# Kernel optimization log

Hardware: AMD Instinct MI355X
Metric: run time of the kernel (lower is better)

The kernel has to match this reference:

```python
import jax, jax.numpy as jnp
import numpy as np

D_MODEL = 1024
N_HEADS = 16
N_GROUPS = 4
D_HEAD = D_MODEL // N_HEADS  # 64
HPG = N_HEADS // N_GROUPS    # heads per KV group = 4
B, T = 2, 2048


def _rope(x):
    # x: [B, H, T, D]; interleaved even/odd rotary, matching the torch module
    t, d = x.shape[2], x.shape[3]
    pos = jnp.arange(t, dtype=jnp.float32)[:, None]                      # [T,1]
    freq = jnp.exp(-(jnp.arange(0, d, 2, dtype=jnp.float32) / d)
                   * jnp.log(jnp.float32(10000.0)))                      # [D/2]
    angle = pos * freq                                                   # [T, D/2]
    cos, sin = jnp.cos(angle), jnp.sin(angle)
    xe, xo = x[..., ::2], x[..., 1::2]
    re = xe * cos - xo * sin
    ro = xe * sin + xo * cos
    return jnp.stack([re, ro], axis=-1).reshape(x.shape)


def setup_inputs() -> dict:
    key = jax.random.key(0)
    ks = jax.random.split(key, 10)
    s = 0.02
    return {
        "x":  jax.random.normal(ks[0], (B, T, D_MODEL), dtype=jnp.float32),
        "Wq": jax.random.normal(ks[1], (D_MODEL, D_MODEL), dtype=jnp.float32) * s,
        "bq": jax.random.normal(ks[2], (D_MODEL,), dtype=jnp.float32) * s,
        "Wk": jax.random.normal(ks[3], (D_MODEL, N_GROUPS * D_HEAD), dtype=jnp.float32) * s,
        "bk": jax.random.normal(ks[4], (N_GROUPS * D_HEAD,), dtype=jnp.float32) * s,
        "Wv": jax.random.normal(ks[5], (D_MODEL, N_GROUPS * D_HEAD), dtype=jnp.float32) * s,
        "bv": jax.random.normal(ks[6], (N_GROUPS * D_HEAD,), dtype=jnp.float32) * s,
        "Wo": jax.random.normal(ks[7], (D_MODEL, D_MODEL), dtype=jnp.float32) * s,
        "bo": jax.random.normal(ks[8], (D_MODEL,), dtype=jnp.float32) * s,
    }


def reference(x, Wq, bq, Wk, bk, Wv, bv, Wo, bo):
    b, t, _ = x.shape
    q = (x @ Wq + bq).reshape(b, t, N_HEADS, D_HEAD).transpose(0, 2, 1, 3)    # [B,H,T,D]
    k = (x @ Wk + bk).reshape(b, t, N_GROUPS, D_HEAD).transpose(0, 2, 1, 3)   # [B,G,T,D]
    v = (x @ Wv + bv).reshape(b, t, N_GROUPS, D_HEAD).transpose(0, 2, 1, 3)
    # GQA broadcast: idx = arange(n_heads) // heads_per_group  ==  repeat each group HPG times
    k = jnp.repeat(k, HPG, axis=1)                                            # [B,H,T,D]
    v = jnp.repeat(v, HPG, axis=1)
    q = _rope(q)
    k = _rope(k)
    scale = jnp.float32(np.sqrt(D_HEAD))
    scores = jnp.einsum('bhtd,bhsd->bhts', q, k) / scale                      # [B,H,T,T]
    causal = jnp.tril(jnp.ones((t, t), dtype=bool))
    scores = jnp.where(causal, scores, -jnp.inf)
    probs = jax.nn.softmax(scores, axis=-1)
    # dropout(p=0.05) is identity in eval mode
    attn = jnp.einsum('bhts,bhsd->bhtd', probs, v)
    out = attn.transpose(0, 2, 1, 3).reshape(b, t, N_HEADS * D_HEAD)
    return out @ Wo + bo
```

## Files before the change

### kernel.cpp

```cpp
#include <hip/hip_runtime.h>
#include <stdint.h>

typedef unsigned short u16;
typedef __attribute__((ext_vector_type(4))) float f32x4;
typedef __attribute__((ext_vector_type(8))) short bf16x8;
typedef __attribute__((ext_vector_type(4))) short bf16x4;

#define T_SEQ 2048
#define DM 1024
#define NH 16
#define NG 4
#define DH 64
#define QSCALE 0.18033688011112042f

__device__ __forceinline__ u16 f2bf(float f) {
    union { float f; uint32_t u; } v; v.f = f;
    uint32_t r = (v.u + 0x7FFFu + ((v.u >> 16) & 1u)) >> 16;
    return (u16)r;
}
__device__ __forceinline__ float bf2f(u16 u) {
    union { uint32_t u; float f; } v; v.u = ((uint32_t)u) << 16;
    return v.f;
}
__device__ __forceinline__ float fexp2(float x) {
#if __has_builtin(__builtin_amdgcn_exp2f)
    return __builtin_amdgcn_exp2f(x);
#else
    return exp2f(x);
#endif
}
__device__ __forceinline__ uint32_t cvtpk_bf16(float a, float b) {
    uint32_t r;
    asm("v_cvt_pk_bf16_f32 %0, %1, %2" : "=v"(r) : "v"(a), "v"(b));
    return r;
}

#if __has_builtin(__builtin_amdgcn_mfma_f32_16x16x16_bf16)
__device__ __forceinline__ f32x4 mfma16(bf16x4 a, bf16x4 b, f32x4 c) {
    return __builtin_amdgcn_mfma_f32_16x16x16_bf16(a, b, c, 0, 0, 0);
}
#elif __has_builtin(__builtin_amdgcn_mfma_f32_16x16x16bf16_1k)
__device__ __forceinline__ f32x4 mfma16(bf16x4 a, bf16x4 b, f32x4 c) {
    return __builtin_amdgcn_mfma_f32_16x16x16bf16_1k(a, b, c, 0, 0, 0);
}
#else
__device__ __forceinline__ f32x4 mfma16(bf16x4 a, bf16x4 b, f32x4 c) {
    asm("v_mfma_f32_16x16x16_bf16 %0, %1, %2, %0" : "+v"(c) : "v"(a), "v"(b));
    return c;
}
#endif

__device__ __forceinline__ void async16(const void* g, void* l) {
    __builtin_amdgcn_global_load_lds(
        (const __attribute__((address_space(1))) void*)g,
        (__attribute__((address_space(3))) void*)l,
        16, 0, 0);
}

__global__ __launch_bounds__(256) void k_prep(
    const float* __restrict__ x, u16* __restrict__ xb,
    const float* __restrict__ Wq, const float* __restrict__ Wk,
    const float* __restrict__ Wv, const float* __restrict__ Wo,
    u16* __restrict__ wqkvt, u16* __restrict__ wot,
    const float* __restrict__ bq, const float* __restrict__ bk,
    const float* __restrict__ bv, float* __restrict__ bqkv,
    float2* __restrict__ tbl) {
    int blk = blockIdx.x;
    int tid = threadIdx.x;
    if (blk < 2048) {
        int i = blk * 256 + tid;
        const float4* p = (const float4*)x + (size_t)i * 2;
        float4 a = p[0], b = p[1];
        bf16x8 v;
        v[0] = (short)f2bf(a.x); v[1] = (short)f2bf(a.y);
        v[2] = (short)f2bf(a.z); v[3] = (short)f2bf(a.w);
        v[4] = (short)f2bf(b.x); v[5] = (short)f2bf(b.y);
        v[6] = (short)f2bf(b.z); v[7] = (short)f2bf(b.w);
        ((bf16x8*)xb)[i] = v;
        return;
    }
    int t = blk - 2048;
    if (t >= 2560) {
        int u = t - 2560;
        if (u < 6) {
            int i = u * 256 + tid;
            if (i < 1536) {
                float v;
                if (i < 1024) v = bq[i];
                else if (i < 1280) v = bk[i - 1024];
                else v = bv[i - 1280];
                bqkv[i] = v;
            }
        } else {
            int idx = (u - 6) * 256 + tid;
            int tt = idx >> 5, i = idx & 31;
            float freq = exp2f(-(float)i * (13.287712379549449f / 32.0f));
            float ang = (float)tt * freq;
            tbl[idx] = make_float2(cosf(ang), sinf(ang));
        }
        return;
    }
    const float* src; u16* dst; int N;
    if (t < 1024)      { src = Wq; dst = wqkvt;                      N = 1024; }
    else if (t < 1280) { t -= 1024; src = Wk; dst = wqkvt + (size_t)1024 * 1024; N = 256; }
    else if (t < 1536) { t -= 1280; src = Wv; dst = wqkvt + (size_t)1280 * 1024; N = 256; }
    else               { t -= 1536; src = Wo; dst = wot;             N = 1024; }
    int ntiles = N >> 5;
    int n0 = (t % ntiles) * 32, k0 = (t / ntiles) * 32;
    __shared__ float tile[32][33];
    int tx = tid & 31, ty = tid >> 5;
#pragma unroll
    for (int q = 0; q < 4; q++)
        tile[ty + q * 8][tx] = src[(size_t)(k0 + ty + q * 8) * N + n0 + tx];
    __syncthreads();
#pragma unroll
    for (int q = 0; q < 4; q++)
        dst[(size_t)(n0 + ty + q * 8) * 1024 + k0 + tx] = f2bf(tile[tx][ty + q * 8]);
}

__global__ __launch_bounds__(256) void k_gemm_qkv(
    const u16* __restrict__ A, const u16* __restrict__ Bt,
    const float* __restrict__ bias, const float2* __restrict__ tbl,
    u16* __restrict__ Qo, u16* __restrict__ Ko, u16* __restrict__ Vto) {
    const int K = 1024;
    __shared__ __align__(16) u16 As[64 * 64];
    __shared__ __align__(16) u16 Bs[128 * 64];
    int tid = threadIdx.x;
    int lane = tid & 63, wid = tid >> 6;
    int wr = wid >> 1, wc = wid & 1;
    int l15 = lane & 15, lhi = lane >> 4;
    int row0 = blockIdx.y * 64, col0 = blockIdx.x * 128;
    f32x4 acc[2][4] = {};

    for (int k0 = 0; k0 < K; k0 += 64) {
#pragma unroll
        for (int i = 0; i < 2; i++) {
            int c = i * 256 + tid;
            int r = c >> 3, ch = c & 7;
            int sch = ch ^ (r & 7);
            async16(A + (size_t)(row0 + r) * K + k0 + sch * 8, &As[c * 8]);
        }
#pragma unroll
        for (int i = 0; i < 4; i++) {
            int c = i * 256 + tid;
            int r = c >> 3, ch = c & 7;
            int sch = ch ^ (r & 7);
            async16(Bt + (size_t)(col0 + r) * K + k0 + sch * 8, &Bs[c * 8]);
        }
        __syncthreads();
#pragma unroll
        for (int ks = 0; ks < 2; ks++) {
            bf16x8 af[2], bfr[4];
#pragma unroll
            for (int m = 0; m < 2; m++) {
                int r = wr * 32 + m * 16 + l15;
                int kb = (ks * 64 + lhi * 16) ^ ((r & 7) << 4);
                af[m] = *(const bf16x8*)((const char*)As + r * 128 + kb);
            }
#pragma unroll
            for (int n = 0; n < 4; n++) {
                int r = wc * 64 + n * 16 + l15;
                int kb = (ks * 64 + lhi * 16) ^ ((r & 7) << 4);
                bfr[n] = *(const bf16x8*)((const char*)Bs + r * 128 + kb);
            }
#pragma unroll
            for (int m = 0; m < 2; m++)
#pragma unroll
                for (int n = 0; n < 4; n++)
                    acc[m][n] = __builtin_amdgcn_mfma_f32_16x16x32_bf16(
                        af[m], bfr[n], acc[m][n], 0, 0, 0);
        }
        __syncthreads();
    }

    int type = (col0 >= 1280) ? 2 : (col0 >= 1024 ? 1 : 0);
    int rbase = row0 + wr * 32;
#pragma unroll
    for (int n = 0; n < 4; n++) {
        int col = col0 + wc * 64 + n * 16 + l15;
        float bv = bias[col];
        if (type == 2) {
            int cc = col - 1280;
            int g = cc >> 6, d = cc & 63;
#pragma unroll
            for (int m = 0; m < 2; m++)
#pragma unroll
                for (int i = 0; i < 4; i++) {
                    int rowg = rbase + m * 16 + lhi * 4 + i;
                    int t = rowg & (T_SEQ - 1), b = rowg >> 11;
                    int sp = t ^ ((d & 1) << 2);
                    Vto[(((size_t)(b * NG + g)) * DH + d) * T_SEQ + sp] =
                        f2bf(acc[m][n][i] + bv);
                }
        } else {
            float ssgn = (col & 1) ? 1.f : -1.f;
            int ip = (col & 63) >> 1;
#pragma unroll
            for (int m = 0; m < 2; m++)
#pragma unroll
                for (int i = 0; i < 4; i++) {
                    int rowg = rbase + m * 16 + lhi * 4 + i;
                    int t = rowg & (T_SEQ - 1), b = rowg >> 11;
                    float v = acc[m][n][i] + bv;
                    float other = __shfl_xor(v, 1);
                    float2 cs = tbl[t * 32 + ip];
                    float out = v * cs.x + other * cs.y * ssgn;
                    if (type == 0) {
                        int h = col >> 6, d = col & 63;
                        Qo[(((size_t)(b * NH + h)) * T_SEQ + t) * DH + d] =
                            f2bf(out * QSCALE);
                    } else {
                        int cc = col - 1024;
                        int g = cc >> 6, d = cc & 63;
                        Ko[(((size_t)(b * NG + g)) * T_SEQ + t) * DH + d] = f2bf(out);
                    }
                }
        }
    }
}

__global__ __launch_bounds__(256) void k_gemm_out(
    const u16* __restrict__ A, const u16* __restrict__ Bt,
    const float* __restrict__ bias, float* __restrict__ C,
    int M, int N, int K) {
    __shared__ __align__(16) u16 As[64 * 64];
    __shared__ __align__(16) u16 Bs[128 * 64];
    int tid = threadIdx.x;
    int lane = tid & 63, wid = tid >> 6;
    int wr = wid >> 1, wc = wid & 1;
    int l15 = lane & 15, lhi = lane >> 4;
    int row0 = blockIdx.y * 64, col0 = blockIdx.x * 128;
    f32x4 acc[2][4] = {};

    for (int k0 = 0; k0 < K; k0 += 64) {
#pragma unroll
        for (int i = 0; i < 2; i++) {
            int c = i * 256 + tid;
            int r = c >> 3, ch = c & 7;
            int sch = ch ^ (r & 7);
            async16(A + (size_t)(row0 + r) * K + k0 + sch * 8, &As[c * 8]);
        }
#pragma unroll
        for (int i = 0; i < 4; i++) {
            int c = i * 256 + tid;
            int r = c >> 3, ch = c & 7;
            int sch = ch ^ (r & 7);
            async16(Bt + (size_t)(col0 + r) * K + k0 + sch * 8, &Bs[c * 8]);
        }
        __syncthreads();
#pragma unroll
        for (int ks = 0; ks < 2; ks++) {
            bf16x8 af[2], bfr[4];
#pragma unroll
            for (int m = 0; m < 2; m++) {
                int r = wr * 32 + m * 16 + l15;
                int kb = (ks * 64 + lhi * 16) ^ ((r & 7) << 4);
                af[m] = *(const bf16x8*)((const char*)As + r * 128 + kb);
            }
#pragma unroll
            for (int n = 0; n < 4; n++) {
                int r = wc * 64 + n * 16 + l15;
                int kb = (ks * 64 + lhi * 16) ^ ((r & 7) << 4);
                bfr[n] = *(const bf16x8*)((const char*)Bs + r * 128 + kb);
            }
#pragma unroll
            for (int m = 0; m < 2; m++)
#pragma unroll
                for (int n = 0; n < 4; n++)
                    acc[m][n] = __builtin_amdgcn_mfma_f32_16x16x32_bf16(
                        af[m], bfr[n], acc[m][n], 0, 0, 0);
        }
        __syncthreads();
    }
#pragma unroll
    for (int n = 0; n < 4; n++) {
        int col = col0 + wc * 64 + n * 16 + l15;
        float bv = bias[col];
#pragma unroll
        for (int m = 0; m < 2; m++) {
            int row = row0 + wr * 32 + m * 16 + lhi * 4;
#pragma unroll
            for (int i = 0; i < 4; i++)
                C[(size_t)(row + i) * N + col] = acc[m][n][i] + bv;
        }
    }
}

__global__ __launch_bounds__(256) void k_attn(
    const u16* __restrict__ Q, const u16* __restrict__ K,
    const u16* __restrict__ Vt, u16* __restrict__ Aout) {
    int i0 = blockIdx.x;
    int u = i0 >> 5;
    int qt = (u < 16) ? (31 - u) : (u - 16);
    int bh = i0 & 31;
    int b = bh >> 4, h = bh & 15, g = h >> 2;
    int tid = threadIdx.x;
    int lane = tid & 63, wid = tid >> 6;
    int l15 = lane & 15, lhi = lane >> 4;

    const u16* Kp = K + ((size_t)(b * NG + g)) * T_SEQ * DH;
    const u16* Vp = Vt + ((size_t)(b * NG + g)) * DH * T_SEQ;

    __shared__ __align__(16) u16 Ks[2][64 * 64];
    __shared__ __align__(16) u16 Vs[2][64 * 64];

    const u16* Qp = Q + ((size_t)bh * T_SEQ + qt * 64) * DH;
    bf16x8 qf[2];
#pragma unroll
    for (int ks = 0; ks < 2; ks++)
        qf[ks] = *(const bf16x8*)(Qp + (size_t)(wid * 16 + l15) * DH + ks * 32 + lhi * 8);

    f32x4 of[4] = {};
    float m_i = -3.0e38f, l_i = 0.f;

    int nt = qt + 1;
    int swz = (l15 & 7) << 4;

    int c0 = tid, c1 = tid + 256;
    int rk0 = c0 >> 3, rk1 = c1 >> 3;
    int sk0 = (c0 & 7) ^ (rk0 & 7);
    int sk1 = (c1 & 7) ^ (rk1 & 7);
    int sv0 = (c0 & 7) ^ ((rk0 >> 1) & 7);
    int sv1 = (c1 & 7) ^ ((rk1 >> 1) & 7);
    const u16* kg0 = Kp + rk0 * DH + sk0 * 8;
    const u16* kg1 = Kp + rk1 * DH + sk1 * 8;
    const u16* vg0 = Vp + (size_t)rk0 * T_SEQ + sv0 * 8;
    const u16* vg1 = Vp + (size_t)rk1 * T_SEQ + sv1 * 8;

    async16(kg0, &Ks[0][c0 * 8]);
    async16(kg1, &Ks[0][c1 * 8]);
    async16(vg0, &Vs[0][c0 * 8]);
    async16(vg1, &Vs[0][c1 * 8]);
    __syncthreads();

#pragma unroll 1
    for (int it = 0; it < nt; it++) {
        int cur = it & 1;
        if (it + 1 < nt) {
            int nx = cur ^ 1;
            int ko = (it + 1) << 12;
            int vo = (it + 1) << 6;
            async16(kg0 + ko, &Ks[nx][c0 * 8]);
            async16(kg1 + ko, &Ks[nx][c1 * 8]);
            async16(vg0 + vo, &Vs[nx][c0 * 8]);
            async16(vg1 + vo, &Vs[nx][c1 * 8]);
        }
        const u16* Kc = Ks[cur];
        const u16* Vc = Vs[cur];

        f32x4 sf[4] = {};
        __builtin_amdgcn_s_setprio(1);
#pragma unroll
        for (int ks = 0; ks < 2; ks++)
#pragma unroll
            for (int n = 0; n < 4; n++) {
                int kb = (ks * 64 + lhi * 16) ^ swz;
                bf16x8 kf = *(const bf16x8*)((const char*)Kc + (n * 16 + l15) * 128 + kb);
                sf[n] = __builtin_amdgcn_mfma_f32_16x16x32_bf16(kf, qf[ks], sf[n], 0, 0, 0);
            }
        __builtin_amdgcn_s_setprio(0);

        if (it == nt - 1) {
            int qrow = qt * 64 + wid * 16 + l15;
            int sb = it * 64 + lhi * 4;
#pragma unroll
            for (int n = 0; n < 4; n++)
#pragma unroll
                for (int i = 0; i < 4; i++)
                    if (sb + n * 16 + i > qrow) sf[n][i] = -3.0e38f;
        }

        float pmt = sf[0][0];
#pragma unroll
        for (int n = 0; n < 4; n++)
#pragma unroll
            for (int i = 0; i < 4; i++)
                pmt = fmaxf(pmt, sf[n][i]);
        if (!__all(pmt - m_i <= 8.f)) {
#pragma unroll
            for (int off = 16; off <= 32; off <<= 1)
                pmt = fmaxf(pmt, __shfl_xor(pmt, off));
            float mn = fmaxf(m_i, pmt);
            float sc = fexp2(m_i - mn);
            m_i = mn;
            l_i *= sc;
            float sc4[4];
#pragma unroll
            for (int i = 0; i < 4; i++)
                sc4[i] = __shfl(sc, lhi * 4 + i);
#pragma unroll
            for (int n = 0; n < 4; n++)
#pragma unroll
                for (int i = 0; i < 4; i++)
                    of[n][i] *= sc4[i];
        }
        bf16x4 pa[4];
#pragma unroll
        for (int n = 0; n < 4; n++) {
#pragma unroll
            for (int i = 0; i < 4; i++) {
                float p = fexp2(sf[n][i] - m_i);
                sf[n][i] = p;
                l_i += p;
            }
            union { uint32_t u[2]; bf16x4 v; } pu;
            pu.u[0] = cvtpk_bf16(sf[n][0], sf[n][1]);
            pu.u[1] = cvtpk_bf16(sf[n][2], sf[n][3]);
            pa[n] = pu.v;
        }

        __builtin_amdgcn_s_setprio(1);
#pragma unroll
        for (int nd = 0; nd < 4; nd++) {
            int rowb = (nd * 16 + l15) * 128;
#pragma unroll
            for (int n = 0; n < 4; n++) {
                int kb = ((4 * n + lhi) ^ l15) << 3;
                bf16x4 vf = *(const bf16x4*)((const char*)Vc + rowb + kb);
                of[nd] = mfma16(pa[n], vf, of[nd]);
            }
        }
        __builtin_amdgcn_s_setprio(0);
        __syncthreads();
    }

#pragma unroll
    for (int off = 16; off <= 32; off <<= 1)
        l_i += __shfl_xor(l_i, off);
    float lq[4];
#pragma unroll
    for (int i = 0; i < 4; i++)
        lq[i] = __shfl(l_i, lhi * 4 + i);
#pragma unroll
    for (int n = 0; n < 4; n++)
#pragma unroll
        for (int i = 0; i < 4; i++) {
            int trow = qt * 64 + wid * 16 + lhi * 4 + i;
            float v = of[n][i] / lq[i];
            Aout[((size_t)(b * T_SEQ + trow)) * DM + h * 64 + n * 16 + l15] = f2bf(v);
        }
}

extern "C" void kernel_launch(void* const* d_in, const int* in_sizes, int n_in,
                              void* d_out, int out_size, void* d_ws, size_t ws_size,
                              hipStream_t stream) {
    const float* x  = (const float*)d_in[0];
    const float* Wq = (const float*)d_in[1];
    const float* bq = (const float*)d_in[2];
    const float* Wk = (const float*)d_in[3];
    const float* bk = (const float*)d_in[4];
    const float* Wv = (const float*)d_in[5];
    const float* bv = (const float*)d_in[6];
    const float* Wo = (const float*)d_in[7];
    const float* bo = (const float*)d_in[8];

    char* ws = (char*)d_ws;
    size_t o = 0;
    u16*   xb    = (u16*)(ws + o);  o += (size_t)4096 * 1024 * 2;
    u16*   wqkvt = (u16*)(ws + o);  o += (size_t)1536 * 1024 * 2;
    u16*   wot   = (u16*)(ws + o);  o += (size_t)1024 * 1024 * 2;
    float* bqkv  = (float*)(ws + o); o += 1536 * 4;
    o = (o + 255) & ~(size_t)255;
    u16*   Qb    = (u16*)(ws + o);  o += (size_t)2 * NH * T_SEQ * DH * 2;
    u16*   Kb    = (u16*)(ws + o);  o += (size_t)2 * NG * T_SEQ * DH * 2;
    u16*   Vtb   = (u16*)(ws + o);  o += (size_t)2 * NG * DH * T_SEQ * 2;
    u16*   attnb = (u16*)(ws + o);  o += (size_t)4096 * 1024 * 2;
    float2* tbl  = (float2*)(ws + o); o += (size_t)2048 * 32 * 8;

    k_prep<<<4870, 256, 0, stream>>>(x, xb, Wq, Wk, Wv, Wo, wqkvt, wot, bq, bk, bv, bqkv, tbl);
    k_gemm_qkv<<<dim3(12, 64), 256, 0, stream>>>(xb, wqkvt, bqkv, tbl, Qb, Kb, Vtb);
    k_attn<<<1024, 256, 0, stream>>>(Qb, Kb, Vtb, attnb);
    k_gemm_out<<<dim3(8, 64), 256, 0, stream>>>(attnb, wot, bo, (float*)d_out, 4096, 1024, 1024);
}
```

Baseline: 91.30 us.

## Double-buffer LDS tiles in projection GEMMs and unify them into one template

The QKV and output projection GEMMs are merged into one templated kernel, with the epilogue chosen by a template parameter. The main loop now double-buffers the A and B shared-memory tiles: the next K-tile's async global-to-LDS copies are issued before the MFMA work on the current tile, so load latency overlaps compute. Global source pointers are also precomputed once, outside the loop. In exchange, shared memory per block doubles, which may lower occupancy. The attention kernel only gets a variable rename.

```diff
diff --git a/kernel.cpp b/kernel.cpp
--- a/kernel.cpp
+++ b/kernel.cpp
@@ -118,13 +118,14 @@
         dst[(size_t)(n0 + ty + q * 8) * 1024 + k0 + tx] = f2bf(tile[tx][ty + q * 8]);
 }
 
-__global__ __launch_bounds__(256) void k_gemm_qkv(
+template <int EPI>
+__global__ __launch_bounds__(256) void k_gemm(
     const u16* __restrict__ A, const u16* __restrict__ Bt,
-    const float* __restrict__ bias, const float2* __restrict__ tbl,
-    u16* __restrict__ Qo, u16* __restrict__ Ko, u16* __restrict__ Vto) {
-    const int K = 1024;
-    __shared__ __align__(16) u16 As[64 * 64];
-    __shared__ __align__(16) u16 Bs[128 * 64];
+    const float* __restrict__ bias, float* __restrict__ C,
+    const float2* __restrict__ tbl, u16* __restrict__ Qo,
+    u16* __restrict__ Ko, u16* __restrict__ Vto, int N, int K) {
+    __shared__ __align__(16) u16 As[2][64 * 64];
+    __shared__ __align__(16) u16 Bs[2][128 * 64];
     int tid = threadIdx.x;
     int lane = tid & 63, wid = tid >> 6;
     int wr = wid >> 1, wc = wid & 1;
@@ -132,22 +133,37 @@
     int row0 = blockIdx.y * 64, col0 = blockIdx.x * 128;
     f32x4 acc[2][4] = {};
 
-    for (int k0 = 0; k0 < K; k0 += 64) {
-#pragma unroll
-        for (int i = 0; i < 2; i++) {
-            int c = i * 256 + tid;
-            int r = c >> 3, ch = c & 7;
-            int sch = ch ^ (r & 7);
-            async16(A + (size_t)(row0 + r) * K + k0 + sch * 8, &As[c * 8]);
-        }
-#pragma unroll
-        for (int i = 0; i < 4; i++) {
-            int c = i * 256 + tid;
-            int r = c >> 3, ch = c & 7;
-            int sch = ch ^ (r & 7);
-            async16(Bt + (size_t)(col0 + r) * K + k0 + sch * 8, &Bs[c * 8]);
-        }
-        __syncthreads();
+    const u16* ga[2];
+    const u16* gb[4];
+#pragma unroll
+    for (int i = 0; i < 2; i++) {
+        int c = i * 256 + tid, r = c >> 3, sch = (c & 7) ^ (r & 7);
+        ga[i] = A + (size_t)(row0 + r) * K + sch * 8;
+    }
+#pragma unroll
+    for (int i = 0; i < 4; i++) {
+        int c = i * 256 + tid, r = c >> 3, sch = (c & 7) ^ (r & 7);
+        gb[i] = Bt + (size_t)(col0 + r) * K + sch * 8;
+    }
+
+#pragma unroll
+    for (int i = 0; i < 2; i++) async16(ga[i], &As[0][(i * 256 + tid) * 8]);
+#pragma unroll
+    for (int i = 0; i < 4; i++) async16(gb[i], &Bs[0][(i * 256 + tid) * 8]);
+    __syncthreads();
+
+    int nk = K >> 6;
+    for (int kt = 0; kt < nk; kt++) {
+        int cur = kt & 1;
+        if (kt + 1 < nk) {
+            int nx = cur ^ 1, ko = (kt + 1) << 6;
+#pragma unroll
+            for (int i = 0; i < 2; i++) async16(ga[i] + ko, &As[nx][(i * 256 + tid) * 8]);
+#pragma unroll
+            for (int i = 0; i < 4; i++) async16(gb[i] + ko, &Bs[nx][(i * 256 + tid) * 8]);
+        }
+        const u16* Ac = As[cur];
+        const u16* Bc = Bs[cur];
 #pragma unroll
         for (int ks = 0; ks < 2; ks++) {
             bf16x8 af[2], bfr[4];
@@ -155,13 +171,13 @@
             for (int m = 0; m < 2; m++) {
                 int r = wr * 32 + m * 16 + l15;
                 int kb = (ks * 64 + lhi * 16) ^ ((r & 7) << 4);
-                af[m] = *(const bf16x8*)((const char*)As + r * 128 + kb);
+                af[m] = *(const bf16x8*)((const char*)Ac + r * 128 + kb);
             }
 #pragma unroll
             for (int n = 0; n < 4; n++) {
                 int r = wc * 64 + n * 16 + l15;
                 int kb = (ks * 64 + lhi * 16) ^ ((r & 7) << 4);
-                bfr[n] = *(const bf16x8*)((const char*)Bs + r * 128 + kb);
+                bfr[n] = *(const bf16x8*)((const char*)Bc + r * 128 + kb);
             }
 #pragma unroll
             for (int m = 0; m < 2; m++)
@@ -173,115 +189,63 @@
         __syncthreads();
     }
 
-    int type = (col0 >= 1280) ? 2 : (col0 >= 1024 ? 1 : 0);
-    int rbase = row0 + wr * 32;
-#pragma unroll
-    for (int n = 0; n < 4; n++) {
-        int col = col0 + wc * 64 + n * 16 + l15;
-        float bv = bias[col];
-        if (type == 2) {
-            int cc = col - 1280;
-            int g = cc >> 6, d = cc & 63;
-#pragma unroll
-            for (int m = 0; m < 2; m++)
-#pragma unroll
-                for (int i = 0; i < 4; i++) {
-                    int rowg = rbase + m * 16 + lhi * 4 + i;
-                    int t = rowg & (T_SEQ - 1), b = rowg >> 11;
-                    int sp = t ^ ((d & 1) << 2);
-                    Vto[(((size_t)(b * NG + g)) * DH + d) * T_SEQ + sp] =
-                        f2bf(acc[m][n][i] + bv);
-                }
-        } else {
-            float ssgn = (col & 1) ? 1.f : -1.f;
-            int ip = (col & 63) >> 1;
-#pragma unroll
-            for (int m = 0; m < 2; m++)
-#pragma unroll
-                for (int i = 0; i < 4; i++) {
-                    int rowg = rbase + m * 16 + lhi * 4 + i;
-                    int t = rowg & (T_SEQ - 1), b = rowg >> 11;
-                    float v = acc[m][n][i] + bv;
-                    float other = __shfl_xor(v, 1);
-                    float2 cs = tbl[t * 32 + ip];
-                    float out = v * cs.x + other * cs.y * ssgn;
-                    if (type == 0) {
-                        int h = col >> 6, d = col & 63;
-                        Qo[(((size_t)(b * NH + h)) * T_SEQ + t) * DH + d] =
-                            f2bf(out * QSCALE);
-                    } else {
-                        int cc = col - 1024;
-                        int g = cc >> 6, d = cc & 63;
-                        Ko[(((size_t)(b * NG + g)) * T_SEQ + t) * DH + d] = f2bf(out);
+    if (EPI == 0) {
+#pragma unroll
+        for (int n = 0; n < 4; n++) {
+            int col = col0 + wc * 64 + n * 16 + l15;
+            float bv = bias[col];
+#pragma unroll
+            for (int m = 0; m < 2; m++) {
+                int row = row0 + wr * 32 + m * 16 + lhi * 4;
+#pragma unroll
+                for (int i = 0; i < 4; i++)
+                    C[(size_t)(row + i) * N + col] = acc[m][n][i] + bv;
+            }
+        }
+    } else {
+        int type = (col0 >= 1280) ? 2 : (col0 >= 1024 ? 1 : 0);
+        int rbase = row0 + wr * 32;
+#pragma unroll
+        for (int n = 0; n < 4; n++) {
+            int col = col0 + wc * 64 + n * 16 + l15;
+            float bv = bias[col];
+            if (type == 2) {
+                int cc = col - 1280;
+                int g = cc >> 6, d = cc & 63;
+#pragma unroll
+                for (int m = 0; m < 2; m++)
+#pragma unroll
+                    for (int i = 0; i < 4; i++) {
+                        int rowg = rbase + m * 16 + lhi * 4 + i;
+                        int t = rowg & (T_SEQ - 1), b = rowg >> 11;
+                        int sp = t ^ ((d & 1) << 2);
+                        Vto[(((size_t)(b * NG + g)) * DH + d) * T_SEQ + sp] =
+                            f2bf(acc[m][n][i] + bv);
                     }
-                }
-        }
-    }
-}
-
-__global__ __launch_bounds__(256) void k_gemm_out(
-    const u16* __restrict__ A, const u16* __restrict__ Bt,
-    const float* __restrict__ bias, float* __restrict__ C,
-    int M, int N, int K) {
-    __shared__ __align__(16) u16 As[64 * 64];
-    __shared__ __align__(16) u16 Bs[128 * 64];
-    int tid = threadIdx.x;
-    int lane = tid & 63, wid = tid >> 6;
-    int wr = wid >> 1, wc = wid & 1;
-    int l15 = lane & 15, lhi = lane >> 4;
-    int row0 = blockIdx.y * 64, col0 = blockIdx.x * 128;
-    f32x4 acc[2][4] = {};
-
-    for (int k0 = 0; k0 < K; k0 += 64) {
-#pragma unroll
-        for (int i = 0; i < 2; i++) {
-            int c = i * 256 + tid;
-            int r = c >> 3, ch = c & 7;
-            int sch = ch ^ (r & 7);
-            async16(A + (size_t)(row0 + r) * K + k0 + sch * 8, &As[c * 8]);
-        }
-#pragma unroll
-        for (int i = 0; i < 4; i++) {
-            int c = i * 256 + tid;
-            int r = c >> 3, ch = c & 7;
-            int sch = ch ^ (r & 7);
-            async16(Bt + (size_t)(col0 + r) * K + k0 + sch * 8, &Bs[c * 8]);
-        }
-        __syncthreads();
-#pragma unroll
-        for (int ks = 0; ks < 2; ks++) {
-            bf16x8 af[2], bfr[4];
-#pragma unroll
-            for (int m = 0; m < 2; m++) {
-                int r = wr * 32 + m * 16 + l15;
-                int kb = (ks * 64 + lhi * 16) ^ ((r & 7) << 4);
-                af[m] = *(const bf16x8*)((const char*)As + r * 128 + kb);
-            }
-#pragma unroll
-            for (int n = 0; n < 4; n++) {
-                int r = wc * 64 + n * 16 + l15;
-                int kb = (ks * 64 + lhi * 16) ^ ((r & 7) << 4);
-                bfr[n] = *(const bf16x8*)((const char*)Bs + r * 128 + kb);
-            }
-#pragma unroll
-            for (int m = 0; m < 2; m++)
-#pragma unroll
-                for (int n = 0; n < 4; n++)
-                    acc[m][n] = __builtin_amdgcn_mfma_f32_16x16x32_bf16(
-                        af[m], bfr[n], acc[m][n], 0, 0, 0);
-        }
-        __syncthreads();
-    }
-#pragma unroll
-    for (int n = 0; n < 4; n++) {
-        int col = col0 + wc * 64 + n * 16 + l15;
-        float bv = bias[col];
-#pragma unroll
-        for (int m = 0; m < 2; m++) {
-            int row = row0 + wr * 32 + m * 16 + lhi * 4;
-#pragma unroll
-            for (int i = 0; i < 4; i++)
-                C[(size_t)(row + i) * N + col] = acc[m][n][i] + bv;
+            } else {
+                float ssgn = (col & 1) ? 1.f : -1.f;
+                int ip = (col & 63) >> 1;
+#pragma unroll
+                for (int m = 0; m < 2; m++)
+#pragma unroll
+                    for (int i = 0; i < 4; i++) {
+                        int rowg = rbase + m * 16 + lhi * 4 + i;
+                        int t = rowg & (T_SEQ - 1), b = rowg >> 11;
+                        float v = acc[m][n][i] + bv;
+                        float other = __shfl_xor(v, 1);
+                        float2 cs = tbl[t * 32 + ip];
+                        float out = v * cs.x + other * cs.y * ssgn;
+                        if (type == 0) {
+                            int h = col >> 6, d = col & 63;
+                            Qo[(((size_t)(b * NH + h)) * T_SEQ + t) * DH + d] =
+                                f2bf(out * QSCALE);
+                        } else {
+                            int cc = col - 1024;
+                            int g = cc >> 6, d = cc & 63;
+                            Ko[(((size_t)(b * NG + g)) * T_SEQ + t) * DH + d] = f2bf(out);
+                        }
+                    }
+            }
         }
     }
 }
@@ -403,9 +367,9 @@
                 sf[n][i] = p;
                 l_i += p;
             }
-            union { uint32_t u[2]; bf16x4 v; } pu;
-            pu.u[0] = cvtpk_bf16(sf[n][0], sf[n][1]);
-            pu.u[1] = cvtpk_bf16(sf[n][2], sf[n][3]);
+            union { uint32_t uu[2]; bf16x4 v; } pu;
+            pu.uu[0] = cvtpk_bf16(sf[n][0], sf[n][1]);
+            pu.uu[1] = cvtpk_bf16(sf[n][2], sf[n][3]);
             pa[n] = pu.v;
         }
 
@@ -468,7 +432,7 @@
     float2* tbl  = (float2*)(ws + o); o += (size_t)2048 * 32 * 8;
 
     k_prep<<<4870, 256, 0, stream>>>(x, xb, Wq, Wk, Wv, Wo, wqkvt, wot, bq, bk, bv, bqkv, tbl);
-    k_gemm_qkv<<<dim3(12, 64), 256, 0, stream>>>(xb, wqkvt, bqkv, tbl, Qb, Kb, Vtb);
+    k_gemm<1><<<dim3(12, 64), 256, 0, stream>>>(xb, wqkvt, bqkv, nullptr, tbl, Qb, Kb, Vtb, 1536, 1024);
     k_attn<<<1024, 256, 0, stream>>>(Qb, Kb, Vtb, attnb);
-    k_gemm_out<<<dim3(8, 64), 256, 0, stream>>>(attnb, wot, bo, (float*)d_out, 4096, 1024, 1024);
-}
+    k_gemm<0><<<dim3(8, 64), 256, 0, stream>>>(attnb, wot, bo, (float*)d_out, nullptr, nullptr, nullptr, nullptr, 1024, 1024);
+}
```

Measured after the change: 90.98 us. No clear change (-0.4%).
